# Performance work log

Hardware: AMD Instinct MI355X
Metric: run time of the kernel (lower is better)

## Reference

```python
import jax, jax.numpy as jnp
import numpy as np

G = 128            # grid_size (hardcoded in NeRFRenderer.__init__)
T = 32             # time_size (reduced from 64 to keep working set < 4GB)
CAS = 1            # cascade = 1 + ceil(log2(bound)), bound = 1
DECAY = 0.95
DENSITY_SCALE = 1.0
DENSITY_THRESH = 0.01


def _expand_bits(v):
    # instant-ngp style 10-bit -> 30-bit expansion (works for 7-bit coords of G=128)
    v = (v * jnp.uint32(0x00010001)) & jnp.uint32(0xFF0000FF)
    v = (v * jnp.uint32(0x00000101)) & jnp.uint32(0x0F00F00F)
    v = (v * jnp.uint32(0x00000011)) & jnp.uint32(0xC30C30C3)
    v = (v * jnp.uint32(0x00000005)) & jnp.uint32(0x49249249)
    return v


def _morton3d(coords):
    # coords: [N, 3] int32 in [0, G)
    x = _expand_bits(coords[:, 0].astype(jnp.uint32))
    y = _expand_bits(coords[:, 1].astype(jnp.uint32))
    z = _expand_bits(coords[:, 2].astype(jnp.uint32))
    return (x | (y << 1) | (z << 2)).astype(jnp.int32)


def setup_inputs() -> dict:
    key = jax.random.key(0)
    k1, k2 = jax.random.split(key)
    density_grid = jax.random.normal(k1, (T, CAS, G ** 3), dtype=jnp.float32) * 0.5
    sigmas = jax.random.uniform(k2, (T, CAS, G ** 3), dtype=jnp.float32)
    return {"density_grid": density_grid, "sigmas": sigmas}


def reference(density_grid, sigmas):
    # full-grid branch of update_extra_state (iter_density < 16)
    g = jnp.arange(G, dtype=jnp.int32)
    xx, yy, zz = jnp.meshgrid(g, g, g, indexing='ij')
    coords = jnp.stack([xx.ravel(), yy.ravel(), zz.ravel()], axis=-1)  # [G^3, 3]
    indices = _morton3d(coords)                                        # [G^3]

    # tmp_grid = -1; tmp_grid[t, cas, indices] = sigmas * density_scale
    tmp_grid = -jnp.ones_like(density_grid)
    tmp_grid = tmp_grid.at[:, :, indices].set(sigmas * DENSITY_SCALE)

    # decay / max merge on mutually-valid cells
    valid = (density_grid >= 0) & (tmp_grid >= 0)
    new_grid = jnp.where(valid, jnp.maximum(density_grid * DECAY, tmp_grid), density_grid)

    # threshold + packbits into bitfield (8 cells per byte, morton order)
    mean_density = jnp.mean(jnp.clip(new_grid, 0.0))
    thresh = jnp.minimum(mean_density, jnp.float32(DENSITY_THRESH))
    bits = (new_grid > thresh).reshape(T, -1, 8)                       # [T, CAS*G^3/8, 8]
    weights = (jnp.int32(1) << jnp.arange(8, dtype=jnp.int32))
    bitfield = jnp.sum(bits.astype(jnp.int32) * weights, axis=-1)      # [T, CAS*G^3/8]
    return new_grid, bitfield
```

## Files before the change

kernel.cpp:

```cpp
#include <hip/hip_runtime.h>

#define G    128
#define G3   (G * G * G)
#define TDIM 32
#define NTOT (TDIM * G3)
#define NBYTES_OUT (NTOT / 8)
#define DECAY 0.95f
#define DTH   0.01f
#define NBLK1 (TDIM * 512)

typedef float f32x4 __attribute__((ext_vector_type(4)));
typedef float f32x2 __attribute__((ext_vector_type(2)));

__device__ __forceinline__ unsigned expand3(unsigned v) {
    v = (v * 0x00010001u) & 0xFF0000FFu;
    v = (v * 0x00000101u) & 0x0F00F00Fu;
    v = (v * 0x00000011u) & 0xC30C30C3u;
    v = (v * 0x00000005u) & 0x49249249u;
    return v;
}
__device__ __forceinline__ unsigned compact3(unsigned v) {
    v &= 0x49249249u;
    v = (v | (v >> 2))  & 0xC30C30C3u;
    v = (v | (v >> 4))  & 0x0F00F00Fu;
    v = (v | (v >> 8))  & 0xFF0000FFu;
    v = (v | (v >> 16)) & 0x000003FFu;
    return v;
}
__device__ __forceinline__ int swz(int m) {
    return (((m >> 7) & 1) << 2) ^ (((m >> 8) & 1) << 3) ^ (((m >> 10) & 1) << 4);
}

__device__ __forceinline__ f32x4 merge4(f32x4 v, f32x4 s) {
    f32x4 r;
    r.x = (v.x >= 0.f && s.x >= 0.f) ? fmaxf(v.x * DECAY, s.x) : v.x;
    r.y = (v.y >= 0.f && s.y >= 0.f) ? fmaxf(v.y * DECAY, s.y) : v.y;
    r.z = (v.z >= 0.f && s.z >= 0.f) ? fmaxf(v.z * DECAY, s.z) : v.z;
    r.w = (v.w >= 0.f && s.w >= 0.f) ? fmaxf(v.w * DECAY, s.w) : v.w;
    return r;
}

__global__ __launch_bounds__(256, 6) void
pass1(const float* __restrict__ dg, const float* __restrict__ sg,
      float* __restrict__ out_grid, float* __restrict__ out_bits,
      float* __restrict__ partials)
{
    __shared__ float smem[4096];
    __shared__ float wsum[4];
    const int blk  = blockIdx.x;
    const int t    = blk >> 9;
    const int cube = blk & 511;
    const int base = t * G3;
    const int tid  = threadIdx.x;
    const int jg0  = base + (cube << 12) + (tid << 4);

    const f32x4* dgp = reinterpret_cast<const f32x4*>(dg + jg0);
    const f32x4 v0 = dgp[0];
    const f32x4 v1 = dgp[1];
    const f32x4 v2 = dgp[2];
    const f32x4 v3 = dgp[3];

    const unsigned Xc = compact3((unsigned)cube);
    const unsigned Yc = compact3((unsigned)cube >> 1);
    const unsigned Zc = compact3((unsigned)cube >> 2);
    const float* __restrict__ sgt = sg + base + (int)((Xc << 18) | (Yc << 11) | (Zc << 4));
    #pragma unroll
    for (int k = 0; k < 4; ++k) {
        const int c  = tid + (k << 8);
        const int lx = c >> 6;
        const int ly = (c >> 2) & 15;
        const int lz = (c & 3) << 2;
        const f32x4 s = *reinterpret_cast<const f32x4*>(sgt + (lx << 14) + (ly << 7) + lz);
        const int m  = (int)(expand3((unsigned)lx) | (expand3((unsigned)ly) << 1)
                           | (expand3((unsigned)lz) << 2));
        const int mb = m ^ swz(m);
        smem[mb]      = s.x;
        smem[mb ^ 4]  = s.y;
        smem[mb ^ 32] = s.z;
        smem[mb ^ 36] = s.w;
    }
    __syncthreads();

    const int j = tid << 4;
    const int b = j ^ swz(j);
    const f32x4 s0 = *reinterpret_cast<const f32x4*>(&smem[b]);
    const f32x4 s1 = *reinterpret_cast<const f32x4*>(&smem[b ^ 4]);
    const f32x4 s2 = *reinterpret_cast<const f32x4*>(&smem[b ^ 8]);
    const f32x4 s3 = *reinterpret_cast<const f32x4*>(&smem[b ^ 12]);

    const f32x4 r0 = merge4(v0, s0);
    const f32x4 r1 = merge4(v1, s1);
    const f32x4 r2 = merge4(v2, s2);
    const f32x4 r3 = merge4(v3, s3);

    f32x4* ogp = reinterpret_cast<f32x4*>(out_grid + jg0);
    ogp[0] = r0;
    ogp[1] = r1;
    ogp[2] = r2;
    ogp[3] = r3;

    float lsum = fmaxf(r0.x, 0.f) + fmaxf(r0.y, 0.f) + fmaxf(r0.z, 0.f) + fmaxf(r0.w, 0.f)
               + fmaxf(r1.x, 0.f) + fmaxf(r1.y, 0.f) + fmaxf(r1.z, 0.f) + fmaxf(r1.w, 0.f)
               + fmaxf(r2.x, 0.f) + fmaxf(r2.y, 0.f) + fmaxf(r2.z, 0.f) + fmaxf(r2.w, 0.f)
               + fmaxf(r3.x, 0.f) + fmaxf(r3.y, 0.f) + fmaxf(r3.z, 0.f) + fmaxf(r3.w, 0.f);

    const int byte0 = (r0.x > DTH ? 1 : 0)  | (r0.y > DTH ? 2 : 0)  |
                      (r0.z > DTH ? 4 : 0)  | (r0.w > DTH ? 8 : 0)  |
                      (r1.x > DTH ? 16 : 0) | (r1.y > DTH ? 32 : 0) |
                      (r1.z > DTH ? 64 : 0) | (r1.w > DTH ? 128 : 0);
    const int byte1 = (r2.x > DTH ? 1 : 0)  | (r2.y > DTH ? 2 : 0)  |
                      (r2.z > DTH ? 4 : 0)  | (r2.w > DTH ? 8 : 0)  |
                      (r3.x > DTH ? 16 : 0) | (r3.y > DTH ? 32 : 0) |
                      (r3.z > DTH ? 64 : 0) | (r3.w > DTH ? 128 : 0);
    f32x2 bb; bb.x = (float)byte0; bb.y = (float)byte1;
    *reinterpret_cast<f32x2*>(out_bits + (jg0 >> 3)) = bb;

    #pragma unroll
    for (int off = 32; off; off >>= 1) lsum += __shfl_down(lsum, off, 64);
    if ((tid & 63) == 0) wsum[tid >> 6] = lsum;
    __syncthreads();
    if (tid == 0)
        partials[blk] = wsum[0] + wsum[1] + wsum[2] + wsum[3];
}

__global__ __launch_bounds__(1024) void
reduce_thresh(const float* __restrict__ partials, float* __restrict__ thresh)
{
    float s = 0.f;
    for (int i = threadIdx.x; i < NBLK1; i += 1024) s += partials[i];
    #pragma unroll
    for (int off = 32; off; off >>= 1) s += __shfl_down(s, off, 64);
    __shared__ float wsum[16];
    if ((threadIdx.x & 63) == 0) wsum[threadIdx.x >> 6] = s;
    __syncthreads();
    if (threadIdx.x == 0) {
        float tot = 0.f;
        #pragma unroll
        for (int i = 0; i < 16; ++i) tot += wsum[i];
        thresh[0] = fminf(tot / (float)NTOT, DTH);
    }
}

__global__ __launch_bounds__(256) void
fix_bits(const float* __restrict__ grid, const float* __restrict__ thresh,
         float* __restrict__ out_bits)
{
    const float th = thresh[0];
    if (th == DTH) return;
    const int n = blockIdx.x * 256 + threadIdx.x;
    const float4* g = reinterpret_cast<const float4*>(grid) + (n << 1);
    const float4 a = g[0], b = g[1];
    int byte = (a.x > th ? 1 : 0)   | (a.y > th ? 2 : 0)   |
               (a.z > th ? 4 : 0)   | (a.w > th ? 8 : 0)   |
               (b.x > th ? 16 : 0)  | (b.y > th ? 32 : 0)  |
               (b.z > th ? 64 : 0)  | (b.w > th ? 128 : 0);
    out_bits[n] = (float)byte;
}

extern "C" void kernel_launch(void* const* d_in, const int* in_sizes, int n_in,
                              void* d_out, int out_size, void* d_ws, size_t ws_size,
                              hipStream_t stream)
{
    const float* dg = (const float*)d_in[0];
    const float* sg = (const float*)d_in[1];
    float* out_grid = (float*)d_out;
    float* out_bits = out_grid + NTOT;
    float* partials = (float*)d_ws;
    float* thresh   = partials + NBLK1;

    pass1<<<NBLK1, 256, 0, stream>>>(dg, sg, out_grid, out_bits, partials);
    reduce_thresh<<<1, 1024, 0, stream>>>(partials, thresh);
    fix_bits<<<NBYTES_OUT / 256, 256, 0, stream>>>(out_grid, thresh, out_bits);
}
```

Measured before the change: 180.5 us.

## Pair z-adjacent Morton cubes per block and grid-stride fix_bits

Each pass1 block now handles two Morton sub-cubes that are adjacent in z, using 512 threads and an 8192-float shared tile. The sigmas gather reads 32 contiguous floats per row instead of 16, which should improve coalescing of the transposed read, and the launch has half as many blocks. fix_bits switches to a fixed 1024-block grid-stride loop, so an early exit costs fewer block launches. The larger shared tile and 512-thread blocks may reduce occupancy.

```diff
diff --git a/kernel.cpp b/kernel.cpp
--- a/kernel.cpp
+++ b/kernel.cpp
@@ -7,7 +7,7 @@
 #define NBYTES_OUT (NTOT / 8)
 #define DECAY 0.95f
 #define DTH   0.01f
-#define NBLK1 (TDIM * 512)
+#define NBLK  (TDIM * 256)
 
 typedef float f32x4 __attribute__((ext_vector_type(4)));
 typedef float f32x2 __attribute__((ext_vector_type(2)));
@@ -40,19 +40,24 @@
     return r;
 }
 
-__global__ __launch_bounds__(256, 6) void
+__global__ __launch_bounds__(512, 8) void
 pass1(const float* __restrict__ dg, const float* __restrict__ sg,
       float* __restrict__ out_grid, float* __restrict__ out_bits,
       float* __restrict__ partials)
 {
-    __shared__ float smem[4096];
-    __shared__ float wsum[4];
+    __shared__ float smem[8192];
+    __shared__ float wsum[8];
     const int blk  = blockIdx.x;
-    const int t    = blk >> 9;
-    const int cube = blk & 511;
+    const int t    = blk >> 8;
+    const int pp   = blk & 255;
+    const int c0   = ((pp >> 2) << 3) | (pp & 3);
     const int base = t * G3;
     const int tid  = threadIdx.x;
-    const int jg0  = base + (cube << 12) + (tid << 4);
+
+    const int cu   = tid >> 8;
+    const int off  = (tid & 255) << 4;
+    const int cube = c0 | (cu << 2);
+    const int jg0  = base + (cube << 12) + off;
 
     const f32x4* dgp = reinterpret_cast<const f32x4*>(dg + jg0);
     const f32x4 v0 = dgp[0];
@@ -60,20 +65,21 @@
     const f32x4 v2 = dgp[2];
     const f32x4 v3 = dgp[3];
 
-    const unsigned Xc = compact3((unsigned)cube);
-    const unsigned Yc = compact3((unsigned)cube >> 1);
-    const unsigned Zc = compact3((unsigned)cube >> 2);
+    const unsigned Xc = compact3((unsigned)c0);
+    const unsigned Yc = compact3((unsigned)c0 >> 1);
+    const unsigned Zc = compact3((unsigned)c0 >> 2);
     const float* __restrict__ sgt = sg + base + (int)((Xc << 18) | (Yc << 11) | (Zc << 4));
     #pragma unroll
     for (int k = 0; k < 4; ++k) {
-        const int c  = tid + (k << 8);
-        const int lx = c >> 6;
-        const int ly = (c >> 2) & 15;
-        const int lz = (c & 3) << 2;
+        const int c   = tid + (k << 9);
+        const int lx  = c >> 7;
+        const int ly  = (c >> 3) & 15;
+        const int lz  = (c & 7) << 2;
         const f32x4 s = *reinterpret_cast<const f32x4*>(sgt + (lx << 14) + (ly << 7) + lz);
-        const int m  = (int)(expand3((unsigned)lx) | (expand3((unsigned)ly) << 1)
-                           | (expand3((unsigned)lz) << 2));
-        const int mb = m ^ swz(m);
+        const int cs  = (lz >> 4) << 12;
+        const int m   = (int)(expand3((unsigned)lx) | (expand3((unsigned)ly) << 1)
+                            | (expand3((unsigned)(lz & 15)) << 2));
+        const int mb  = cs + (m ^ swz(m));
         smem[mb]      = s.x;
         smem[mb ^ 4]  = s.y;
         smem[mb ^ 32] = s.z;
@@ -81,8 +87,7 @@
     }
     __syncthreads();
 
-    const int j = tid << 4;
-    const int b = j ^ swz(j);
+    const int b = (cu << 12) + (off ^ swz(off));
     const f32x4 s0 = *reinterpret_cast<const f32x4*>(&smem[b]);
     const f32x4 s1 = *reinterpret_cast<const f32x4*>(&smem[b ^ 4]);
     const f32x4 s2 = *reinterpret_cast<const f32x4*>(&smem[b ^ 8]);
@@ -116,18 +121,22 @@
     *reinterpret_cast<f32x2*>(out_bits + (jg0 >> 3)) = bb;
 
     #pragma unroll
-    for (int off = 32; off; off >>= 1) lsum += __shfl_down(lsum, off, 64);
+    for (int offl = 32; offl; offl >>= 1) lsum += __shfl_down(lsum, offl, 64);
     if ((tid & 63) == 0) wsum[tid >> 6] = lsum;
     __syncthreads();
-    if (tid == 0)
-        partials[blk] = wsum[0] + wsum[1] + wsum[2] + wsum[3];
+    if (tid == 0) {
+        float tot = 0.f;
+        #pragma unroll
+        for (int i = 0; i < 8; ++i) tot += wsum[i];
+        partials[blk] = tot;
+    }
 }
 
 __global__ __launch_bounds__(1024) void
 reduce_thresh(const float* __restrict__ partials, float* __restrict__ thresh)
 {
     float s = 0.f;
-    for (int i = threadIdx.x; i < NBLK1; i += 1024) s += partials[i];
+    for (int i = threadIdx.x; i < NBLK; i += 1024) s += partials[i];
     #pragma unroll
     for (int off = 32; off; off >>= 1) s += __shfl_down(s, off, 64);
     __shared__ float wsum[16];
@@ -147,14 +156,15 @@
 {
     const float th = thresh[0];
     if (th == DTH) return;
-    const int n = blockIdx.x * 256 + threadIdx.x;
-    const float4* g = reinterpret_cast<const float4*>(grid) + (n << 1);
-    const float4 a = g[0], b = g[1];
-    int byte = (a.x > th ? 1 : 0)   | (a.y > th ? 2 : 0)   |
-               (a.z > th ? 4 : 0)   | (a.w > th ? 8 : 0)   |
-               (b.x > th ? 16 : 0)  | (b.y > th ? 32 : 0)  |
-               (b.z > th ? 64 : 0)  | (b.w > th ? 128 : 0);
-    out_bits[n] = (float)byte;
+    for (int n = blockIdx.x * 256 + threadIdx.x; n < NBYTES_OUT; n += 256 * 1024) {
+        const float4* g = reinterpret_cast<const float4*>(grid) + (n << 1);
+        const float4 a = g[0], b = g[1];
+        int byte = (a.x > th ? 1 : 0)   | (a.y > th ? 2 : 0)   |
+                   (a.z > th ? 4 : 0)   | (a.w > th ? 8 : 0)   |
+                   (b.x > th ? 16 : 0)  | (b.y > th ? 32 : 0)  |
+                   (b.z > th ? 64 : 0)  | (b.w > th ? 128 : 0);
+        out_bits[n] = (float)byte;
+    }
 }
 
 extern "C" void kernel_launch(void* const* d_in, const int* in_sizes, int n_in,
@@ -166,9 +176,9 @@
     float* out_grid = (float*)d_out;
     float* out_bits = out_grid + NTOT;
     float* partials = (float*)d_ws;
-    float* thresh   = partials + NBLK1;
+    float* thresh   = partials + NBLK;
 
-    pass1<<<NBLK1, 256, 0, stream>>>(dg, sg, out_grid, out_bits, partials);
+    pass1<<<NBLK, 512, 0, stream>>>(dg, sg, out_grid, out_bits, partials);
     reduce_thresh<<<1, 1024, 0, stream>>>(partials, thresh);
-    fix_bits<<<NBYTES_OUT / 256, 256, 0, stream>>>(out_grid, thresh, out_bits);
+    fix_bits<<<1024, 256, 0, stream>>>(out_grid, thresh, out_bits);
 }
```

After: 165.8 us. -8.2%, faster.
